# Performance work log

Measured on AMD Instinct MI355X. Metric: run time of the kernel, lower is better.

## Reference

```python
import jax, jax.numpy as jnp
import numpy as np

B, S, D, H = 8, 2048, 256, 4
HD = D // H  # 64
EPS = 1e-5


def setup_inputs() -> dict:
    key = jax.random.key(0)
    ks = jax.random.split(key, 16)
    sc = 0.05
    return {
        "descriptors": jax.random.normal(ks[0], (B, S, D), jnp.float32),
        "source": jax.random.normal(ks[1], (B, S, D), jnp.float32),
        "mask": jnp.ones((B, S), jnp.int32),
        # attention projections (stored as [in, out])
        "q_w": jax.random.normal(ks[2], (D, D), jnp.float32) * sc,
        "q_b": jnp.zeros((D,), jnp.float32),
        "k_w": jax.random.normal(ks[3], (D, D), jnp.float32) * sc,
        "k_b": jnp.zeros((D,), jnp.float32),
        "v_w": jax.random.normal(ks[4], (D, D), jnp.float32) * sc,
        "v_b": jnp.zeros((D,), jnp.float32),
        "o_w": jax.random.normal(ks[5], (D, D), jnp.float32) * sc,
        "o_b": jnp.zeros((D,), jnp.float32),
        # MLP layer 0: 2D -> 2D, BatchNorm1d (eval mode) + ReLU
        "m0_w": jax.random.normal(ks[6], (2 * D, 2 * D), jnp.float32) * sc,
        "m0_b": jnp.zeros((2 * D,), jnp.float32),
        "bn_g": jax.random.uniform(ks[7], (2 * D,), jnp.float32, 0.5, 1.5),
        "bn_b": jax.random.normal(ks[8], (2 * D,), jnp.float32) * 0.1,
        "bn_m": jax.random.normal(ks[9], (2 * D,), jnp.float32) * 0.1,
        "bn_v": jax.random.uniform(ks[10], (2 * D,), jnp.float32, 0.5, 1.5),
        # MLP layer 1: 2D -> D, no activation
        "m1_w": jax.random.normal(ks[11], (2 * D, D), jnp.float32) * sc,
        "m1_b": jnp.zeros((D,), jnp.float32),
    }


def reference(descriptors, source, mask, q_w, q_b, k_w, k_b, v_w, v_b, o_w, o_b,
              m0_w, m0_b, bn_g, bn_b, bn_m, bn_v, m1_w, m1_b):
    # Multi-head cross-attention: query=descriptors, key=value=source
    q = (descriptors @ q_w + q_b).reshape(B, S, H, HD).transpose(0, 2, 1, 3)  # [B,H,S,HD]
    k = (source @ k_w + k_b).reshape(B, S, H, HD).transpose(0, 2, 1, 3)
    v = (source @ v_w + v_b).reshape(B, S, H, HD).transpose(0, 2, 1, 3)

    scores = jnp.einsum("bhqd,bhkd->bhqk", q, k) / jnp.sqrt(jnp.float32(HD))
    scores = jnp.where(mask[:, None, None, :] == 0, -1e9, scores)
    probs = jax.nn.softmax(scores.astype(jnp.float32), axis=-1)  # [B,H,S,S]

    ctx = jnp.einsum("bhqk,bhkd->bhqd", probs, v)  # [B,H,S,HD]
    ctx = ctx.transpose(0, 2, 1, 3).reshape(B, S, D)
    attn_out = ctx @ o_w + o_b  # out_proj

    # concat + MLP (Linear -> BatchNorm1d(eval) -> ReLU -> Linear)
    h = jnp.concatenate([descriptors, attn_out], axis=-1)  # [B,S,2D]
    h = h @ m0_w + m0_b
    h = (h - bn_m) * jax.lax.rsqrt(bn_v + EPS) * bn_g + bn_b  # per-channel BN
    h = jax.nn.relu(h)
    h = h @ m1_w + m1_b  # [B,S,D]
    return h
```

## Files before the change

kernel.cpp:

```cpp
#include <hip/hip_runtime.h>

#define NB 8
#define NS 2048
#define ND 256
#define NH 4
#define NHD 64
#define ND2 512
#define NM (NB * NS)
#define C1 0.18033688f

typedef __attribute__((ext_vector_type(8))) short          bf16x8;
typedef __attribute__((ext_vector_type(4))) float          f32x4;
typedef __attribute__((ext_vector_type(16))) float         f32x16;
typedef unsigned short ushort_t;
typedef unsigned int   uint_t;

#define MFMA16(a, b, c) __builtin_amdgcn_mfma_f32_16x16x32_bf16(a, b, c, 0, 0, 0)
#define MFMA32(a, b, c) __builtin_amdgcn_mfma_f32_32x32x16_bf16(a, b, c, 0, 0, 0)

#if __has_builtin(__builtin_amdgcn_exp2f)
#define EXP2(x) __builtin_amdgcn_exp2f(x)
#else
#define EXP2(x) exp2f(x)
#endif

static __device__ inline uint_t pack2bf(float a, float b) {
    union { float f; uint_t u; } x, y; x.f = a; y.f = b;
    return __builtin_amdgcn_perm(y.u + 0x8000u, x.u + 0x8000u, 0x07060302u);
}
static __device__ inline ushort_t f2bf(float f) {
    union { float f; uint_t u; } x; x.f = f;
    return (ushort_t)((x.u + 0x7FFFu + ((x.u >> 16) & 1u)) >> 16);
}
static __device__ inline uint_t cvtpk_bf16(float a, float b) {
    uint_t r;
    asm("v_cvt_pk_bf16_f32 %0, %1, %2" : "=v"(r) : "v"(a), "v"(b));
    return r;
}
static __device__ inline void plswap(uint_t &a, uint_t &b) {
    asm("v_permlane32_swap_b32 %0, %1" : "+v"(a), "+v"(b));
}


static __device__ inline void femit(ushort_t* buf, int n, int k, float v) {
    const int kc = k >> 5;
    const int lane = (((k >> 3) & 3) << 4) | (n & 15);
    const int j = k & 7;
    buf[((size_t)(((n >> 4) * 16 + kc) * 64 + lane)) * 8 + j] = f2bf(v);
}

__global__ __launch_bounds__(256) void prep(
    const float* __restrict__ desc, const float* __restrict__ srcp,
    const int* __restrict__ mask,
    const float* __restrict__ q_w, const float* __restrict__ k_w,
    const float* __restrict__ v_w, const float* __restrict__ m1_w,
    const float* __restrict__ o_w, const float* __restrict__ o_b,
    const float* __restrict__ m0_w, const float* __restrict__ m0_b,
    const float* __restrict__ bng, const float* __restrict__ bnb,
    const float* __restrict__ bnm, const float* __restrict__ bnv,
    ushort_t* __restrict__ descF, ushort_t* __restrict__ srcF,
    ushort_t* __restrict__ qwF, ushort_t* __restrict__ kwF,
    ushort_t* __restrict__ vwF, ushort_t* __restrict__ m1F,
    ushort_t* __restrict__ m0fF, float* __restrict__ biasf,
    float* __restrict__ mbias)
{
    __shared__ float ow[256];
    const int blk = blockIdx.x;
    const int t = threadIdx.x;

    if (blk < 4096) {
        const int y = blk >> 11, x = blk & 2047;
        const float* src = y ? srcp : desc;
        ushort_t* dst    = y ? srcF : descF;
        const int g = x * 256 + t;
        const int lane = g & 63, ci = g >> 6;
        const int kc = ci & 7, r16 = ci >> 3;
        const int row = r16 * 16 + (lane & 15);
        const int c0  = kc * 32 + (lane >> 4) * 8;
        const float* p = src + (size_t)row * ND + c0;
        float4 a = *(const float4*)p;
        float4 b = *(const float4*)(p + 4);
        uint4 pk;
        pk.x = pack2bf(a.x, a.y); pk.y = pack2bf(a.z, a.w);
        pk.z = pack2bf(b.x, b.y); pk.w = pack2bf(b.z, b.w);
        *(uint4*)(dst + (size_t)g * 8) = pk;
    } else if (blk < 4352) {
        const int wb = blk - 4096;
        const int y = wb >> 6, x = wb & 63;
        const float* src; ushort_t* dst; int K, N; float sc = 1.0f;
        switch (y) {
            case 0: src = q_w; dst = qwF; K = 256; N = 256; sc = C1; break;
            case 1: src = k_w; dst = kwF; K = 256; N = 256; break;
            case 2: src = v_w; dst = vwF; K = 256; N = 256; break;
            default: src = m1_w; dst = m1F; K = 512; N = 256; break;
        }
        const int g = x * 256 + t;
        if (g >= (N * K) / 8) return;
        const int lane = g & 63, ci = g >> 6;
        const int lgck = (K == 512) ? 4 : 3;
        const int kc = ci & ((1 << lgck) - 1), n16 = ci >> lgck;
        const int n  = n16 * 16 + (lane & 15);
        const int k0 = kc * 32 + (lane >> 4) * 8;
        float f[8];
#pragma unroll
        for (int j = 0; j < 8; j++) f[j] = src[(size_t)(k0 + j) * N + n] * sc;
        uint4 pk;
        pk.x = pack2bf(f[0], f[1]); pk.y = pack2bf(f[2], f[3]);
        pk.z = pack2bf(f[4], f[5]); pk.w = pack2bf(f[6], f[7]);
        *(uint4*)(dst + (size_t)g * 8) = pk;
    } else if (blk < 4416) {
        const int i = (blk - 4352) * 256 + t;
        mbias[i] = mask[i] ? 0.0f : -1e9f;
    } else if (blk < 4672) {
        const int i = blk - 4416;
        ow[t] = o_w[i * 256 + t];
        __syncthreads();
        float f0 = 0.f, f1 = 0.f;
#pragma unroll 4
        for (int j = 0; j < 256; j++) {
            const float w = ow[j];
            f0 += w * m0_w[(size_t)(256 + j) * 512 + t];
            f1 += w * m0_w[(size_t)(256 + j) * 512 + t + 256];
        }
        const float A0v = bng[t] * rsqrtf(bnv[t] + 1e-5f);
        const float A1v = bng[t + 256] * rsqrtf(bnv[t + 256] + 1e-5f);
        femit(m0fF, t, 256 + i, f0 * A0v);
        femit(m0fF, t + 256, 256 + i, f1 * A1v);
        femit(m0fF, t, i, m0_w[(size_t)i * 512 + t] * A0v);
        femit(m0fF, t + 256, i, m0_w[(size_t)i * 512 + t + 256] * A1v);
    } else {
        const int bb = blk - 4672;
        const int n  = bb * 32 + (t >> 3);
        const int jp = t & 7;
        float s = 0.f;
#pragma unroll 4
        for (int j = jp * 32; j < jp * 32 + 32; j++)
            s += o_b[j] * m0_w[(size_t)(256 + j) * 512 + n];
        s += __shfl_xor(s, 1);
        s += __shfl_xor(s, 2);
        s += __shfl_xor(s, 4);
        if (jp == 0) {
            const float A = bng[n] * rsqrtf(bnv[n] + 1e-5f);
            biasf[n] = (m0_b[n] + s - bnm[n]) * A + bnb[n];
        }
    }
}

template <int KC, int AK, bool NAT, int MT>
static __device__ inline void core(
    const ushort_t* __restrict__ A0, const ushort_t* __restrict__ A1,
    const ushort_t* __restrict__ WF, int t16, int n16, f32x4 acc[MT][4])
{
    const int lane = threadIdx.x & 63;
#pragma unroll
    for (int kc = 0; kc < KC; kc++) {
        const ushort_t* Ab = (kc < AK) ? A0 : A1;
        const int kca = (kc < AK) ? kc : kc - AK;
        bf16x8 af[MT], wf[4];
#pragma unroll
        for (int mt = 0; mt < MT; mt++)
            af[mt] = *(const bf16x8*)(Ab + ((size_t)((t16 + mt) * AK + kca) * 64 + lane) * 8);
#pragma unroll
        for (int nt = 0; nt < 4; nt++)
            wf[nt] = *(const bf16x8*)(WF + ((size_t)((n16 + nt) * KC + kc) * 64 + lane) * 8);
#pragma unroll
        for (int mt = 0; mt < MT; mt++)
#pragma unroll
            for (int nt = 0; nt < 4; nt++) {
                if (NAT) acc[mt][nt] = MFMA16(af[mt], wf[nt], acc[mt][nt]);
                else     acc[mt][nt] = MFMA16(wf[nt], af[mt], acc[mt][nt]);
            }
    }
}

__global__ __launch_bounds__(256) void qkv_frag(
    const ushort_t* __restrict__ descF, const ushort_t* __restrict__ srcF,
    const ushort_t* __restrict__ qwF, const ushort_t* __restrict__ kwF,
    const ushort_t* __restrict__ vwF,
    const float* __restrict__ q_b, const float* __restrict__ k_b,
    const float* __restrict__ v_b,
    ushort_t* __restrict__ qF, ushort_t* __restrict__ kF,
    ushort_t* __restrict__ vF)
{
    const int t = threadIdx.x, w = t >> 6;
    const int lq = t & 15, lg = (t & 63) >> 4;
    const int h    = blockIdx.x;
    const int tok0 = (blockIdx.y << 8) + (w << 6);
    const int t16  = tok0 >> 4, n16 = h << 2;
    const int z    = blockIdx.z;

    f32x4 acc[4][4];
#pragma unroll
    for (int mt = 0; mt < 4; mt++)
#pragma unroll
        for (int nt = 0; nt < 4; nt++) acc[mt][nt] = (f32x4){0.f, 0.f, 0.f, 0.f};

    if (z == 2) {
        core<8, 8, true, 4>(srcF, srcF, vwF, t16, n16, acc);
#pragma unroll
        for (int nt = 0; nt < 4; nt++) {
            const int dvh = nt * 16 + lq;
            const float bs = v_b[h * 64 + dvh];
#pragma unroll
            for (int mt = 0; mt < 4; mt++) {
                const int tok = tok0 + mt * 16 + lg * 4;
                const int b = tok >> 11, s0 = tok & 2047;
                const int bh = b * NH + h;
                uint2 pv;
                pv.x = pack2bf(acc[mt][nt][0] + bs, acc[mt][nt][1] + bs);
                pv.y = pack2bf(acc[mt][nt][2] + bs, acc[mt][nt][3] + bs);
                const size_t e = (size_t)bh * 131072 +
                    ((size_t)((dvh >> 4) * 64 + (s0 >> 5)) * 64 +
                     (((s0 >> 3) & 3) * 16 + (dvh & 15))) * 8 + (s0 & 7);
                *(uint2*)(vF + e) = pv;
            }
        }
    } else {
        const ushort_t* A = z ? srcF : descF;
        const ushort_t* W = z ? kwF : qwF;
        const float* bias = z ? k_b : q_b;
        ushort_t* dst     = z ? kF : qF;
        const float bsc   = z ? 1.0f : C1;
        core<8, 8, false, 4>(A, A, W, t16, n16, acc);
#pragma unroll
        for (int nt = 0; nt < 4; nt++) {
            const int d0 = nt * 16 + lg * 4;
            f32x4 b4 = *(const f32x4*)(bias + h * 64 + d0);
#pragma unroll
            for (int mt = 0; mt < 4; mt++) {
                const int tok = tok0 + mt * 16 + lq;
                const int b = tok >> 11, s = tok & 2047;
                const int bh = b * NH + h;
                uint2 pv;
                pv.x = pack2bf(acc[mt][nt][0] + b4[0] * bsc,
                               acc[mt][nt][1] + b4[1] * bsc);
                pv.y = pack2bf(acc[mt][nt][2] + b4[2] * bsc,
                               acc[mt][nt][3] + b4[3] * bsc);
                const size_t e = (size_t)bh * 131072 +
                    ((size_t)((s >> 4) * 2 + (d0 >> 5)) * 64 +
                     (((d0 >> 3) & 3) * 16 + lq)) * 8 + (d0 & 7);
                *(uint2*)(dst + e) = pv;
            }
        }
    }
}

__global__ __launch_bounds__(256) void mlp0_frag(
    const ushort_t* __restrict__ descF, const ushort_t* __restrict__ ctxF,
    const ushort_t* __restrict__ m0fF, const float* __restrict__ biasf,
    ushort_t* __restrict__ hF)
{
    const int t = threadIdx.x, w = t >> 6;
    const int lq = t & 15, lg = (t & 63) >> 4;
    const int n0   = blockIdx.x << 6;
    const int tok0 = (blockIdx.y << 8) + (w << 6);
    const int t16  = tok0 >> 4, n16 = n0 >> 4;

    f32x4 acc[4][4];
#pragma unroll
    for (int mt = 0; mt < 4; mt++)
#pragma unroll
        for (int nt = 0; nt < 4; nt++) acc[mt][nt] = (f32x4){0.f, 0.f, 0.f, 0.f};

    core<16, 8, false, 4>(descF, ctxF, m0fF, t16, n16, acc);

#pragma unroll
    for (int nt = 0; nt < 4; nt++) {
        const int c0 = n0 + nt * 16 + lg * 4;
        f32x4 b4 = *(const f32x4*)(biasf + c0);
#pragma unroll
        for (int mt = 0; mt < 4; mt++) {
            const int tok = tok0 + mt * 16 + lq;
            uint2 pv;
            pv.x = pack2bf(fmaxf(acc[mt][nt][0] + b4[0], 0.f),
                           fmaxf(acc[mt][nt][1] + b4[1], 0.f));
            pv.y = pack2bf(fmaxf(acc[mt][nt][2] + b4[2], 0.f),
                           fmaxf(acc[mt][nt][3] + b4[3], 0.f));
            const size_t e = ((size_t)((tok >> 4) * 16 + (c0 >> 5)) * 64 +
                              (((c0 >> 3) & 3) * 16 + lq)) * 8 + (c0 & 7);
            *(uint2*)(hF + e) = pv;
        }
    }
}

__global__ __launch_bounds__(256) void mlp1_frag(
    const ushort_t* __restrict__ hF, const ushort_t* __restrict__ m1F,
    const float* __restrict__ m1_b, float* __restrict__ out)
{
    const int t = threadIdx.x, w = t >> 6;
    const int lq = t & 15, lg = (t & 63) >> 4;
    const int n0   = blockIdx.x << 6;
    const int tok0 = (blockIdx.y << 7) + (w << 5);
    const int t16  = tok0 >> 4, n16 = n0 >> 4;

    f32x4 acc[2][4];
#pragma unroll
    for (int mt = 0; mt < 2; mt++)
#pragma unroll
        for (int nt = 0; nt < 4; nt++) acc[mt][nt] = (f32x4){0.f, 0.f, 0.f, 0.f};

    core<16, 16, false, 2>(hF, hF, m1F, t16, n16, acc);

#pragma unroll
    for (int nt = 0; nt < 4; nt++) {
        const int c0 = n0 + nt * 16 + lg * 4;
        f32x4 b4 = *(const f32x4*)(m1_b + c0);
#pragma unroll
        for (int mt = 0; mt < 2; mt++) {
            const int tok = tok0 + mt * 16 + lq;
            f32x4 o4;
#pragma unroll
            for (int j = 0; j < 4; j++) o4[j] = acc[mt][nt][j] + b4[j];
            *(f32x4*)(out + (size_t)tok * ND + c0) = o4;
        }
    }
}

__global__ __launch_bounds__(256) void attn_frag(
    const ushort_t* __restrict__ qF, const ushort_t* __restrict__ kF,
    const ushort_t* __restrict__ vF, const float* __restrict__ mbias,
    ushort_t* __restrict__ ctxF)
{
    __shared__ f32x4 Ob[2][2][4][64];
    __shared__ float Ls[2][64];

    const int t = threadIdx.x, w = t >> 6, lane = t & 63;
    const int wq = w & 1, kw = w >> 1;
    const int q = lane & 31, h = lane >> 5;
    const int flat = blockIdx.x + (blockIdx.y << 5) + (blockIdx.z << 7);
    const int bh = (flat & 7) + (((flat >> 8) & 3) << 3);
    const int qb = (flat >> 3) & 31;

    const ushort_t* qh = qF + (size_t)bh * 131072;
    const ushort_t* kh = kF + (size_t)bh * 131072;
    const ushort_t* vh = vF + (size_t)bh * 131072;
    const float* mrow = mbias + (bh >> 2) * NS;

    const int qrow0 = qb * 64 + wq * 32;
    const int tok = qrow0 + q;
    const int kbase = kw << 10;

    bf16x8 qf[4];
#pragma unroll
    for (int st = 0; st < 4; st++)
        qf[st] = *(const bf16x8*)(qh +
            ((size_t)(((tok >> 4) * 2 + (st >> 1)) * 64 +
                      ((st * 2 + h) & 3) * 16 + (tok & 15))) * 8);

    f32x16 o[2];
#pragma unroll
    for (int dt = 0; dt < 2; dt++)
#pragma unroll
        for (int j = 0; j < 16; j++) o[dt][j] = 0.f;
    float l_part = 0.0f;

    bf16x8 ka[2][4];
#pragma unroll
    for (int kt = 0; kt < 2; kt++)
#pragma unroll
        for (int st = 0; st < 4; st++) {
            const int key = kbase + kt * 32 + q;
            ka[kt][st] = *(const bf16x8*)(kh +
                ((size_t)(((key >> 4) * 2 + (st >> 1)) * 64 +
                          ((st * 2 + h) & 3) * 16 + (key & 15))) * 8);
        }

    for (int k0 = 0; k0 < 1024; k0 += 64) {
        const int key0 = kbase + k0;

        bf16x8 vf[2][4];
#pragma unroll
        for (int dt = 0; dt < 2; dt++)
#pragma unroll
            for (int st = 0; st < 4; st++) {
                const int d = dt * 32 + q;
                vf[dt][st] = *(const bf16x8*)(vh +
                    ((size_t)(((d >> 4) * 64 + (key0 >> 5) + (st >> 1)) * 64 +
                              ((st * 2 + h) & 3) * 16 + (d & 15))) * 8);
            }

        f32x16 sa[2];
#pragma unroll
        for (int kt = 0; kt < 2; kt++)
#pragma unroll
            for (int r1 = 0; r1 < 4; r1++) {
                f32x4 m4 = *(const f32x4*)(mrow + key0 + kt * 32 + r1 * 8 + h * 4);
#pragma unroll
                for (int r0 = 0; r0 < 4; r0++) sa[kt][r1 * 4 + r0] = m4[r0];
            }

        __builtin_amdgcn_s_setprio(1);
#pragma unroll
        for (int kt = 0; kt < 2; kt++)
#pragma unroll
            for (int st = 0; st < 4; st++)
                sa[kt] = MFMA32(ka[kt][st], qf[st], sa[kt]);
        __builtin_amdgcn_s_setprio(0);

        const int keyn = kbase + ((k0 + 64) & 1023);
#pragma unroll
        for (int kt = 0; kt < 2; kt++)
#pragma unroll
            for (int st = 0; st < 4; st++) {
                const int key = keyn + kt * 32 + q;
                ka[kt][st] = *(const bf16x8*)(kh +
                    ((size_t)(((key >> 4) * 2 + (st >> 1)) * 64 +
                              ((st * 2 + h) & 3) * 16 + (key & 15))) * 8);
            }

        uint_t W[2][4][2];
#pragma unroll
        for (int kt = 0; kt < 2; kt++)
#pragma unroll
            for (int r1 = 0; r1 < 4; r1++)
#pragma unroll
                for (int wv = 0; wv < 2; wv++) {
                    const float p0 = EXP2(sa[kt][r1 * 4 + wv * 2]);
                    const float p1 = EXP2(sa[kt][r1 * 4 + wv * 2 + 1]);
                    l_part += p0 + p1;
                    W[kt][r1][wv] = cvtpk_bf16(p0, p1);
                }
#pragma unroll
        for (int kt = 0; kt < 2; kt++)
#pragma unroll
            for (int s1 = 0; s1 < 2; s1++)
#pragma unroll
                for (int wv = 0; wv < 2; wv++)
                    plswap(W[kt][2 * s1][wv], W[kt][2 * s1 + 1][wv]);

        __builtin_amdgcn_s_setprio(1);
#pragma unroll
        for (int st = 0; st < 4; st++) {
            const int kt = st >> 1, s1 = st & 1;
            union { uint_t u[4]; bf16x8 v; } pb;
            pb.u[0] = W[kt][2 * s1][0];
            pb.u[1] = W[kt][2 * s1][1];
            pb.u[2] = W[kt][2 * s1 + 1][0];
            pb.u[3] = W[kt][2 * s1 + 1][1];
#pragma unroll
            for (int dt = 0; dt < 2; dt++)
                o[dt] = MFMA32(vf[dt][st], pb.v, o[dt]);
        }
        __builtin_amdgcn_s_setprio(0);
    }

    l_part += __shfl_xor(l_part, 32);

    if (kw) {
#pragma unroll
        for (int dt = 0; dt < 2; dt++)
#pragma unroll
            for (int r1 = 0; r1 < 4; r1++) {
                f32x4 v;
#pragma unroll
                for (int r0 = 0; r0 < 4; r0++) v[r0] = o[dt][r1 * 4 + r0];
                Ob[wq][dt][r1][lane] = v;
            }
        Ls[wq][lane] = l_part;
    }
    __syncthreads();
    if (kw) return;

    const float li = 1.0f / (l_part + Ls[wq][lane]);

    const int tok16 = (bh >> 2) * 128 + (tok >> 4);
#pragma unroll
    for (int dt = 0; dt < 2; dt++)
#pragma unroll
        for (int r1 = 0; r1 < 4; r1++) {
            const f32x4 p = Ob[wq][dt][r1][lane];
            const int c = (bh & 3) * 64 + dt * 32 + r1 * 8 + h * 4;
            uint2 pv;
            pv.x = cvtpk_bf16((o[dt][r1 * 4 + 0] + p[0]) * li,
                              (o[dt][r1 * 4 + 1] + p[1]) * li);
            pv.y = cvtpk_bf16((o[dt][r1 * 4 + 2] + p[2]) * li,
                              (o[dt][r1 * 4 + 3] + p[3]) * li);
            const size_t e = ((size_t)(tok16 * 8 + (c >> 5)) * 64 +
                              (((c >> 3) & 3) * 16 + (tok & 15))) * 8 + (c & 7);
            *(uint2*)(ctxF + e) = pv;
        }
}

extern "C" void kernel_launch(void* const* d_in, const int* in_sizes, int n_in,
                              void* d_out, int out_size, void* d_ws, size_t ws_size,
                              hipStream_t stream)
{
    (void)in_sizes; (void)n_in; (void)out_size; (void)ws_size;
    const float* desc = (const float*)d_in[0];
    const float* srcp = (const float*)d_in[1];
    const int*   mask = (const int*)d_in[2];
    const float* q_w  = (const float*)d_in[3];
    const float* q_b  = (const float*)d_in[4];
    const float* k_w  = (const float*)d_in[5];
    const float* k_b  = (const float*)d_in[6];
    const float* v_w  = (const float*)d_in[7];
    const float* v_b  = (const float*)d_in[8];
    const float* o_w  = (const float*)d_in[9];
    const float* o_b  = (const float*)d_in[10];
    const float* m0_w = (const float*)d_in[11];
    const float* m0_b = (const float*)d_in[12];
    const float* bng  = (const float*)d_in[13];
    const float* bnb  = (const float*)d_in[14];
    const float* bnm  = (const float*)d_in[15];
    const float* bnv  = (const float*)d_in[16];
    const float* m1_w = (const float*)d_in[17];
    const float* m1_b = (const float*)d_in[18];
    float* out = (float*)d_out;

    const size_t ASZ = (size_t)NM * ND;
    ushort_t* descF = (ushort_t*)d_ws;
    ushort_t* srcF  = descF + ASZ;
    ushort_t* qF    = descF + 2 * ASZ;
    ushort_t* kF    = descF + 3 * ASZ;
    ushort_t* vF    = descF + 4 * ASZ;
    ushort_t* qwF   = descF + 5 * ASZ;
    ushort_t* kwF   = qwF + 65536;
    ushort_t* vwF   = kwF + 65536;
    ushort_t* m1F   = vwF + 65536;
    ushort_t* m0fF  = m1F + 131072;
    float*    biasf = (float*)(m0fF + 262144);
    float*    mbias = biasf + 512;
    ushort_t* ctxF  = srcF;
    ushort_t* hF    = qF;

    const dim3 blk(256);

    prep<<<dim3(4688), blk, 0, stream>>>(
        desc, srcp, mask, q_w, k_w, v_w, m1_w, o_w, o_b, m0_w, m0_b,
        bng, bnb, bnm, bnv, descF, srcF, qwF, kwF, vwF, m1F, m0fF, biasf, mbias);

    qkv_frag<<<dim3(4, NM / 256, 3), blk, 0, stream>>>(
        descF, srcF, qwF, kwF, vwF, q_b, k_b, v_b, qF, kF, vF);
    attn_frag<<<dim3(NS / 64, NH, NB), blk, 0, stream>>>(qF, kF, vF, mbias, ctxF);
    mlp0_frag<<<dim3(8, NM / 256), blk, 0, stream>>>(descF, ctxF, m0fF, biasf, hF);
    mlp1_frag<<<dim3(4, NM / 128), blk, 0, stream>>>(hF, m1F, m1_b, out);
}
```

Before: 243.8 us.

## Pack attention mask into bitwords and branch on fully-unmasked key tiles

The float additive mask is replaced by a 32-bit-per-word key mask built in prep. The attention kernel now starts the score accumulators at zero and, only when a 64-key tile contains a masked key, zeroes the affected probabilities after exp2. This removes the per-tile float4 mask loads from the inner loop. The row-sum accumulation is also split into four partial sums to shorten the dependency chain. The cost is a divergent branch per tile and duplicated softmax code. Fully masked rows now yield zero sums instead of a uniform softmax as with the old -1e9 bias.

```diff
diff --git a/kernel.cpp b/kernel.cpp
--- a/kernel.cpp
+++ b/kernel.cpp
@@ -62,7 +62,7 @@
     ushort_t* __restrict__ qwF, ushort_t* __restrict__ kwF,
     ushort_t* __restrict__ vwF, ushort_t* __restrict__ m1F,
     ushort_t* __restrict__ m0fF, float* __restrict__ biasf,
-    float* __restrict__ mbias)
+    uint_t* __restrict__ mbits)
 {
     __shared__ float ow[256];
     const int blk = blockIdx.x;
@@ -108,11 +108,15 @@
         pk.x = pack2bf(f[0], f[1]); pk.y = pack2bf(f[2], f[3]);
         pk.z = pack2bf(f[4], f[5]); pk.w = pack2bf(f[6], f[7]);
         *(uint4*)(dst + (size_t)g * 8) = pk;
-    } else if (blk < 4416) {
-        const int i = (blk - 4352) * 256 + t;
-        mbias[i] = mask[i] ? 0.0f : -1e9f;
-    } else if (blk < 4672) {
-        const int i = blk - 4416;
+    } else if (blk < 4354) {
+        const int g = (blk - 4352) * 256 + t;
+        const int base = g * 32;
+        uint_t m = 0;
+#pragma unroll
+        for (int j = 0; j < 32; j++) m |= (mask[base + j] ? 1u : 0u) << j;
+        mbits[g] = m;
+    } else if (blk < 4610) {
+        const int i = blk - 4354;
         ow[t] = o_w[i * 256 + t];
         __syncthreads();
         float f0 = 0.f, f1 = 0.f;
@@ -129,7 +133,7 @@
         femit(m0fF, t, i, m0_w[(size_t)i * 512 + t] * A0v);
         femit(m0fF, t + 256, i, m0_w[(size_t)i * 512 + t + 256] * A1v);
     } else {
-        const int bb = blk - 4672;
+        const int bb = blk - 4610;
         const int n  = bb * 32 + (t >> 3);
         const int jp = t & 7;
         float s = 0.f;
@@ -318,7 +322,7 @@
 
 __global__ __launch_bounds__(256) void attn_frag(
     const ushort_t* __restrict__ qF, const ushort_t* __restrict__ kF,
-    const ushort_t* __restrict__ vF, const float* __restrict__ mbias,
+    const ushort_t* __restrict__ vF, const uint_t* __restrict__ mbits,
     ushort_t* __restrict__ ctxF)
 {
     __shared__ f32x4 Ob[2][2][4][64];
@@ -334,7 +338,7 @@
     const ushort_t* qh = qF + (size_t)bh * 131072;
     const ushort_t* kh = kF + (size_t)bh * 131072;
     const ushort_t* vh = vF + (size_t)bh * 131072;
-    const float* mrow = mbias + (bh >> 2) * NS;
+    const uint_t* mw = mbits + (bh >> 2) * 64 + (kw << 5);
 
     const int qrow0 = qb * 64 + wq * 32;
     const int tok = qrow0 + q;
@@ -379,15 +383,14 @@
                               ((st * 2 + h) & 3) * 16 + (d & 15))) * 8);
             }
 
+        const uint_t mw0 = mw[(k0 >> 5)];
+        const uint_t mw1 = mw[(k0 >> 5) + 1];
+
         f32x16 sa[2];
 #pragma unroll
         for (int kt = 0; kt < 2; kt++)
 #pragma unroll
-            for (int r1 = 0; r1 < 4; r1++) {
-                f32x4 m4 = *(const f32x4*)(mrow + key0 + kt * 32 + r1 * 8 + h * 4);
-#pragma unroll
-                for (int r0 = 0; r0 < 4; r0++) sa[kt][r1 * 4 + r0] = m4[r0];
-            }
+            for (int j = 0; j < 16; j++) sa[kt][j] = 0.f;
 
         __builtin_amdgcn_s_setprio(1);
 #pragma unroll
@@ -408,18 +411,40 @@
                               ((st * 2 + h) & 3) * 16 + (key & 15))) * 8);
             }
 
+        float ls0 = 0.f, ls1 = 0.f, ls2 = 0.f, ls3 = 0.f;
         uint_t W[2][4][2];
-#pragma unroll
-        for (int kt = 0; kt < 2; kt++)
-#pragma unroll
-            for (int r1 = 0; r1 < 4; r1++)
-#pragma unroll
-                for (int wv = 0; wv < 2; wv++) {
-                    const float p0 = EXP2(sa[kt][r1 * 4 + wv * 2]);
-                    const float p1 = EXP2(sa[kt][r1 * 4 + wv * 2 + 1]);
-                    l_part += p0 + p1;
-                    W[kt][r1][wv] = cvtpk_bf16(p0, p1);
-                }
+
+#define SMAX_BODY(DM)                                                         \
+        _Pragma("unroll")                                                     \
+        for (int kt = 0; kt < 2; kt++) {                                      \
+            _Pragma("unroll")                                                 \
+            for (int r1 = 0; r1 < 4; r1++) {                                  \
+                _Pragma("unroll")                                             \
+                for (int wv = 0; wv < 2; wv++) {                              \
+                    float p0 = EXP2(sa[kt][r1 * 4 + wv * 2]);                 \
+                    float p1 = EXP2(sa[kt][r1 * 4 + wv * 2 + 1]);             \
+                    if (DM) {                                                 \
+                        const uint_t mk = (kt ? mw1 : mw0) >> (h * 4);        \
+                        if (!((mk >> (r1 * 8 + wv * 2)) & 1u)) p0 = 0.f;      \
+                        if (!((mk >> (r1 * 8 + wv * 2)) & 2u)) p1 = 0.f;      \
+                    }                                                         \
+                    if (kt == 0) { if (wv == 0) ls0 += p0 + p1;               \
+                                   else         ls1 += p0 + p1; }             \
+                    else         { if (wv == 0) ls2 += p0 + p1;               \
+                                   else         ls3 += p0 + p1; }             \
+                    W[kt][r1][wv] = cvtpk_bf16(p0, p1);                       \
+                }                                                             \
+            }                                                                 \
+        }
+
+        if (__builtin_expect((mw0 & mw1) != 0xFFFFFFFFu, 0)) {
+            SMAX_BODY(1)
+        } else {
+            SMAX_BODY(0)
+        }
+#undef SMAX_BODY
+        l_part += (ls0 + ls1) + (ls2 + ls3);
+
 #pragma unroll
         for (int kt = 0; kt < 2; kt++)
 #pragma unroll
@@ -519,19 +544,19 @@
     ushort_t* m1F   = vwF + 65536;
     ushort_t* m0fF  = m1F + 131072;
     float*    biasf = (float*)(m0fF + 262144);
-    float*    mbias = biasf + 512;
+    uint_t*   mbits = (uint_t*)(biasf + 512);
     ushort_t* ctxF  = srcF;
     ushort_t* hF    = qF;
 
     const dim3 blk(256);
 
-    prep<<<dim3(4688), blk, 0, stream>>>(
+    prep<<<dim3(4626), blk, 0, stream>>>(
         desc, srcp, mask, q_w, k_w, v_w, m1_w, o_w, o_b, m0_w, m0_b,
-        bng, bnb, bnm, bnv, descF, srcF, qwF, kwF, vwF, m1F, m0fF, biasf, mbias);
+        bng, bnb, bnm, bnv, descF, srcF, qwF, kwF, vwF, m1F, m0fF, biasf, mbits);
 
     qkv_frag<<<dim3(4, NM / 256, 3), blk, 0, stream>>>(
         descF, srcF, qwF, kwF, vwF, q_b, k_b, v_b, qF, kF, vF);
-    attn_frag<<<dim3(NS / 64, NH, NB), blk, 0, stream>>>(qF, kF, vF, mbias, ctxF);
+    attn_frag<<<dim3(NS / 64, NH, NB), blk, 0, stream>>>(qF, kF, vF, mbits, ctxF);
     mlp0_frag<<<dim3(8, NM / 256), blk, 0, stream>>>(descF, ctxF, m0fF, biasf, hF);
     mlp1_frag<<<dim3(4, NM / 128), blk, 0, stream>>>(hF, m1F, m1_b, out);
 }
```

Result: faster. 237.6 us (-2.5%).
